# Optimization experiments

Hardware: AMD Instinct MI355X
Metric: run time of the kernel (lower is better)

The kernel has to match this reference:

```python
import jax, jax.numpy as jnp
import numpy as np

N_NODES = 50000
N_EDGES = 800000
IN_F = 128
OUT_F = 128
N_LAYERS = 2


def setup_inputs() -> dict:
    key = jax.random.key(0)
    ks = jax.random.split(key, 8)
    x = jax.random.normal(ks[0], (N_NODES, IN_F), dtype=jnp.float32)
    hidden_states = jax.random.normal(ks[1], (N_LAYERS, N_NODES, OUT_F), dtype=jnp.float32)
    src = jax.random.randint(ks[2], (N_EDGES,), 0, N_NODES)
    dst = jax.random.randint(ks[3], (N_EDGES,), 0, N_NODES)
    edge_w = jax.random.uniform(ks[4], (N_EDGES,), dtype=jnp.float32)
    # [layer, gate(r,u,c), in+out, out], scaled like typical init
    W_self = jax.random.normal(ks[5], (N_LAYERS, 3, IN_F + OUT_F, OUT_F), dtype=jnp.float32) * 0.05
    W_neigh = jax.random.normal(ks[6], (N_LAYERS, 3, IN_F + OUT_F, OUT_F), dtype=jnp.float32) * 0.05
    bias = jax.random.uniform(ks[7], (N_LAYERS, 3, OUT_F), dtype=jnp.float32)
    return {"x": x, "hidden_states": hidden_states, "src": src, "dst": dst,
            "edge_w": edge_w, "W_self": W_self, "W_neigh": W_neigh, "bias": bias}


def _gconv(z, src, dst, edge_w, ws, wn):
    # z: [N, 2F]; message passing: sum_{e: dst=v} edge_w[e] * z[src[e]]
    msg = z[src] * edge_w[:, None]                      # [E, 2F]
    agg = jax.ops.segment_sum(msg, dst, num_segments=N_NODES)  # [N, 2F]
    return z @ ws + agg @ wn                            # [N, F]


def _cell(x, h, src, dst, edge_w, ws, wn, b):
    # ws/wn: [3, 2F, F], b: [3, F]; gates r,u,c as in GraphGRUCell
    xh = jnp.concatenate([x, h], axis=1)
    r = jax.nn.sigmoid(_gconv(xh, src, dst, edge_w, ws[0], wn[0]) + b[0])
    u = jax.nn.sigmoid(_gconv(xh, src, dst, edge_w, ws[1], wn[1]) + b[1])
    xh2 = jnp.concatenate([x, r * h], axis=1)
    c = jax.nn.sigmoid(_gconv(xh2, src, dst, edge_w, ws[2], wn[2]) + b[2])
    return u * h + (1.0 - u) * c


def reference(x, hidden_states, src, dst, edge_w, W_self, W_neigh, bias):
    hiddens = []
    for i in range(N_LAYERS):  # small fixed layer count
        x = _cell(x, hidden_states[i], src, dst, edge_w, W_self[i], W_neigh[i], bias[i])
        hiddens.append(x)
    return (x, hiddens)
```

## Files before the change

kernel.cpp:

```cpp
#include <hip/hip_runtime.h>
#include <math.h>

#define F 128
#define NLAYERS 2

typedef __attribute__((ext_vector_type(8))) short bf16x8s;
typedef __attribute__((ext_vector_type(8))) unsigned short u16x8;
typedef __attribute__((ext_vector_type(4))) float f32x4;

__device__ __forceinline__ float sigmoidf_(float x) { return 1.0f / (1.0f + expf(-x)); }

__device__ __forceinline__ unsigned short f2bf(float f) {
    unsigned int u = __float_as_uint(f);
    u += 0x7fffu + ((u >> 16) & 1u);
    return (unsigned short)(u >> 16);
}
__device__ __forceinline__ float bf2f(unsigned short s) {
    return __uint_as_float(((unsigned int)s) << 16);
}

__global__ void pack_w_bf16(const float* __restrict__ Ws, const float* __restrict__ Wn,
                            unsigned short* __restrict__ W1b, unsigned short* __restrict__ W2b) {
    int t = blockIdx.x * blockDim.x + threadIdx.x;
    const int n1 = 2 * 64 * 256 * 8;
    if (t < n1) {
        int j = t & 7, n = (t >> 3) & 255, ko = (t >> 11) & 63, l = t >> 17;
        int k = ko * 8 + j;
        int p = k >> 7, r = k & 127, g = n >> 7, c = n & 127;
        const float* W = (p < 2) ? Ws : Wn;
        W1b[t] = f2bf(W[(((l * 3 + g) * 256) + ((p & 1) * 128 + r)) * 128 + c]);
    } else {
        int t2 = t - n1;
        if (t2 >= 2 * 64 * 128 * 8) return;
        int j = t2 & 7, n = (t2 >> 3) & 127, ko = (t2 >> 10) & 63, l = t2 >> 16;
        int k = ko * 8 + j;
        int p = k >> 7, r = k & 127;
        const float* W = (p < 2) ? Ws : Wn;
        W2b[t2] = f2bf(W[(((l * 3 + 2) * 256) + ((p & 1) * 128 + r)) * 128 + n]);
    }
}

__global__ void cvt_all(const float* __restrict__ x, const float* __restrict__ hidden,
                        unsigned short* __restrict__ xh0, unsigned short* __restrict__ xh1,
                        int n4, size_t NF) {
    int t = blockIdx.x * blockDim.x + threadIdx.x;
    const float* in;
    unsigned short* out;
    int tt;
    if (t < n4) { in = x; out = xh0; tt = t; }
    else if (t < 2 * n4) { in = hidden; out = xh0 + 128; tt = t - n4; }
    else if (t < 3 * n4) { in = hidden + NF; out = xh1 + 128; tt = t - 2 * n4; }
    else return;
    float4 v = reinterpret_cast<const float4*>(in)[tt];
    ushort4 o;
    o.x = f2bf(v.x); o.y = f2bf(v.y); o.z = f2bf(v.z); o.w = f2bf(v.w);
    *reinterpret_cast<ushort4*>(out + (((size_t)(tt >> 5)) << 8) + ((tt & 31) << 2)) = o;
}

__global__ void hist_key(const int* __restrict__ src, const int* __restrict__ dst,
                         int* __restrict__ cnt, int E) {
    int e = blockIdx.x * blockDim.x + threadIdx.x;
    if (e < E) atomicAdd(&cnt[(dst[e] << 4) + (src[e] >> 12)], 1);
}

__global__ __launch_bounds__(1024) void scan_blk(const int* __restrict__ cnt,
                                                 int* __restrict__ offs,
                                                 int* __restrict__ bsum, int n) {
    __shared__ int wsum[16];
    int tid = threadIdx.x, lane = tid & 63, wid = tid >> 6;
    int i = blockIdx.x * 1024 + tid;
    int v = (i < n) ? cnt[i] : 0;
    int incl = v;
#pragma unroll
    for (int off = 1; off < 64; off <<= 1) {
        int t = __shfl_up(incl, off, 64);
        if (lane >= off) incl += t;
    }
    if (lane == 63) wsum[wid] = incl;
    __syncthreads();
    if (wid == 0) {
        int s = (lane < 16) ? wsum[lane] : 0;
#pragma unroll
        for (int off = 1; off < 16; off <<= 1) {
            int t = __shfl_up(s, off, 64);
            if (lane >= off) s += t;
        }
        if (lane < 16) wsum[lane] = s;
    }
    __syncthreads();
    int wbase = (wid > 0) ? wsum[wid - 1] : 0;
    if (i < n) offs[i] = wbase + incl - v;
    if (tid == 1023) bsum[blockIdx.x] = wbase + incl;
}

__global__ __launch_bounds__(1024) void scan_tops(int* __restrict__ bsum, int nb,
                                                  int* __restrict__ total_out) {
    __shared__ int wsum[16];
    int tid = threadIdx.x, lane = tid & 63, wid = tid >> 6;
    int v = (tid < nb) ? bsum[tid] : 0;
    int incl = v;
#pragma unroll
    for (int off = 1; off < 64; off <<= 1) {
        int t = __shfl_up(incl, off, 64);
        if (lane >= off) incl += t;
    }
    if (lane == 63) wsum[wid] = incl;
    __syncthreads();
    if (wid == 0) {
        int s = (lane < 16) ? wsum[lane] : 0;
#pragma unroll
        for (int off = 1; off < 16; off <<= 1) {
            int t = __shfl_up(s, off, 64);
            if (lane >= off) s += t;
        }
        if (lane < 16) wsum[lane] = s;
    }
    __syncthreads();
    int wbase = (wid > 0) ? wsum[wid - 1] : 0;
    if (tid < nb) bsum[tid] = wbase + incl - v;
    if (tid == 1023) *total_out = wbase + incl;
}

__global__ __launch_bounds__(1024) void scan_add(const int* __restrict__ bsum,
                                                 int* __restrict__ offs,
                                                 int* __restrict__ cursor, int n) {
    int i = blockIdx.x * 1024 + threadIdx.x;
    if (i >= n) return;
    int o = offs[i] + bsum[blockIdx.x];
    offs[i] = o;
    cursor[i] = o;
}

__global__ void scatter_edges(const int* __restrict__ src, const int* __restrict__ dst,
                              const float* __restrict__ ew, int* __restrict__ cursor,
                              int2* __restrict__ es, int E) {
    int e = blockIdx.x * blockDim.x + threadIdx.x;
    if (e >= E) return;
    int s = src[e];
    int key = (dst[e] << 4) + (s >> 12);
    int p = atomicAdd(&cursor[key], 1);
    es[p] = make_int2(s, __float_as_int(ew[e]));
}

__global__ __launch_bounds__(256) void agg_csr2_i(
    const unsigned short* __restrict__ XH,
    const int2* __restrict__ es, const int* __restrict__ offs2,
    unsigned short* __restrict__ agg0, unsigned short* __restrict__ agg1, int N) {
    int node = blockIdx.x * 8 + (threadIdx.x >> 5);
    if (node >= N) return;
    int lane = threadIdx.x & 31;
    int beg = offs2[node << 4], end = offs2[(node << 4) + 16];
    float a0[8] = {0, 0, 0, 0, 0, 0, 0, 0};
    float a1[8] = {0, 0, 0, 0, 0, 0, 0, 0};
    int loff = lane << 3;
    int i = beg;
    for (; i + 3 < end; i += 4) {
        int2 e0 = es[i], e1 = es[i + 1], e2 = es[i + 2], e3 = es[i + 3];
        u16x8 v0 = *reinterpret_cast<const u16x8*>(XH + (((size_t)e0.x) << 8) + loff);
        u16x8 v1 = *reinterpret_cast<const u16x8*>(XH + (((size_t)e1.x) << 8) + loff);
        u16x8 v2 = *reinterpret_cast<const u16x8*>(XH + (((size_t)e2.x) << 8) + loff);
        u16x8 v3 = *reinterpret_cast<const u16x8*>(XH + (((size_t)e3.x) << 8) + loff);
        float w0 = __int_as_float(e0.y), w1 = __int_as_float(e1.y);
        float w2 = __int_as_float(e2.y), w3 = __int_as_float(e3.y);
#pragma unroll
        for (int j = 0; j < 8; ++j) {
            a0[j] += w0 * bf2f(v0[j]);
            a1[j] += w1 * bf2f(v1[j]);
            a0[j] += w2 * bf2f(v2[j]);
            a1[j] += w3 * bf2f(v3[j]);
        }
    }
    for (; i < end; ++i) {
        int2 e0 = es[i];
        float w0 = __int_as_float(e0.y);
        u16x8 v0 = *reinterpret_cast<const u16x8*>(XH + (((size_t)e0.x) << 8) + loff);
#pragma unroll
        for (int j = 0; j < 8; ++j) a0[j] += w0 * bf2f(v0[j]);
    }
    u16x8 o;
#pragma unroll
    for (int j = 0; j < 8; ++j) o[j] = f2bf(a0[j] + a1[j]);
    unsigned short* op = (lane < 16)
        ? (agg0 + (((size_t)node) << 7) + (lane << 3))
        : (agg1 + (((size_t)node) << 7) + ((lane & 15) << 3));
    *reinterpret_cast<u16x8*>(op) = o;
}

__global__ __launch_bounds__(256) void agg_csr1_b(
    const unsigned short* __restrict__ V0,
    const int2* __restrict__ es, const int* __restrict__ offs2,
    unsigned short* __restrict__ agg0, int N) {
    int node = blockIdx.x * 8 + (threadIdx.x >> 5);
    if (node >= N) return;
    int lane = threadIdx.x & 31;
    int beg = offs2[node << 4], end = offs2[(node << 4) + 16];
    float p0[4] = {0, 0, 0, 0}, p1[4] = {0, 0, 0, 0};
    int loff = lane << 2;
    int i = beg;
    for (; i + 3 < end; i += 4) {
        int2 e0 = es[i], e1 = es[i + 1], e2 = es[i + 2], e3 = es[i + 3];
        ushort4 x0 = *reinterpret_cast<const ushort4*>(V0 + (((size_t)e0.x) << 7) + loff);
        ushort4 x1 = *reinterpret_cast<const ushort4*>(V0 + (((size_t)e1.x) << 7) + loff);
        ushort4 x2 = *reinterpret_cast<const ushort4*>(V0 + (((size_t)e2.x) << 7) + loff);
        ushort4 x3 = *reinterpret_cast<const ushort4*>(V0 + (((size_t)e3.x) << 7) + loff);
        float w0 = __int_as_float(e0.y), w1 = __int_as_float(e1.y);
        float w2 = __int_as_float(e2.y), w3 = __int_as_float(e3.y);
        p0[0] += w0 * bf2f(x0.x); p0[1] += w0 * bf2f(x0.y);
        p0[2] += w0 * bf2f(x0.z); p0[3] += w0 * bf2f(x0.w);
        p1[0] += w1 * bf2f(x1.x); p1[1] += w1 * bf2f(x1.y);
        p1[2] += w1 * bf2f(x1.z); p1[3] += w1 * bf2f(x1.w);
        p0[0] += w2 * bf2f(x2.x); p0[1] += w2 * bf2f(x2.y);
        p0[2] += w2 * bf2f(x2.z); p0[3] += w2 * bf2f(x2.w);
        p1[0] += w3 * bf2f(x3.x); p1[1] += w3 * bf2f(x3.y);
        p1[2] += w3 * bf2f(x3.z); p1[3] += w3 * bf2f(x3.w);
    }
    for (; i < end; ++i) {
        int2 e0 = es[i];
        float w0 = __int_as_float(e0.y);
        ushort4 x0 = *reinterpret_cast<const ushort4*>(V0 + (((size_t)e0.x) << 7) + loff);
        p0[0] += w0 * bf2f(x0.x); p0[1] += w0 * bf2f(x0.y);
        p0[2] += w0 * bf2f(x0.z); p0[3] += w0 * bf2f(x0.w);
    }
    size_t ob = (((size_t)node) << 7) + loff;
    ushort4 o0;
    o0.x = f2bf(p0[0] + p1[0]); o0.y = f2bf(p0[1] + p1[1]);
    o0.z = f2bf(p0[2] + p1[2]); o0.w = f2bf(p0[3] + p1[3]);
    *reinterpret_cast<ushort4*>(agg0 + ob) = o0;
}

__global__ __launch_bounds__(512) void gemm_ru(
    const unsigned short* __restrict__ XH,
    const unsigned short* __restrict__ AGGX, const unsigned short* __restrict__ AGGH,
    const unsigned short* __restrict__ Wb, const float* __restrict__ bias,
    const float* __restrict__ hfull,
    unsigned short* __restrict__ rhb, float* __restrict__ u, int N) {
    __shared__ __align__(16) unsigned short Als[2][4 * 128 * 8];
    __shared__ __align__(16) unsigned short Bls[2][4 * 128 * 8];

    int tid = threadIdx.x;
    int row0 = blockIdx.x * 128;
    int n0c = blockIdx.y * 128;
    int lane = tid & 63;
    int w = tid >> 6;
    int wrow = (w & 1) << 6;
    int wcol = (w >> 1) << 5;
    int quad = lane >> 4, l16 = lane & 15;

    f32x4 acc[4][2];
    const f32x4 z4 = {0.f, 0.f, 0.f, 0.f};
#pragma unroll
    for (int mt = 0; mt < 4; ++mt)
#pragma unroll
        for (int nt = 0; nt < 2; ++nt) acc[mt][nt] = z4;

    int mA = tid & 127, qA = tid >> 7;
    int growA = row0 + mA;
    if (growA >= N) growA = N - 1;
    int nB = tid & 127, qB = tid >> 7;

    auto stage = [&](int ks, int buf) {
        int p = ks >> 7;
        const unsigned short* ga =
            (p == 0) ? (XH + (size_t)growA * 256 + (ks & 127) + (qA << 3))
          : (p == 1) ? (XH + (size_t)growA * 256 + 128 + (ks & 127) + (qA << 3))
          : (p == 2) ? (AGGX + ((size_t)growA << 7) + (ks & 127) + (qA << 3))
                     : (AGGH + ((size_t)growA << 7) + (ks & 127) + (qA << 3));
        __builtin_amdgcn_global_load_lds(
            (const __attribute__((address_space(1))) void*)ga,
            (__attribute__((address_space(3))) void*)&Als[buf][((qA << 7) + mA) << 3], 16, 0, 0);
        int koG = (ks >> 3) + qB;
        const unsigned short* gb = Wb + ((size_t)(koG * 256 + n0c + nB) << 3);
        __builtin_amdgcn_global_load_lds(
            (const __attribute__((address_space(1))) void*)gb,
            (__attribute__((address_space(3))) void*)&Bls[buf][((qB << 7) + nB) << 3], 16, 0, 0);
    };

    stage(0, 0);
    __syncthreads();
    int buf = 0;
    for (int ks = 0; ks < 512; ks += 32, buf ^= 1) {
        if (ks + 32 < 512) stage(ks + 32, buf ^ 1);

        bf16x8s af[4], bfr[2];
#pragma unroll
        for (int mt = 0; mt < 4; ++mt)
            af[mt] = *reinterpret_cast<const bf16x8s*>(
                &Als[buf][((quad << 7) + wrow + (mt << 4) + l16) << 3]);
#pragma unroll
        for (int nt = 0; nt < 2; ++nt)
            bfr[nt] = *reinterpret_cast<const bf16x8s*>(
                &Bls[buf][((quad << 7) + wcol + (nt << 4) + l16) << 3]);
#pragma unroll
        for (int mt = 0; mt < 4; ++mt)
#pragma unroll
            for (int nt = 0; nt < 2; ++nt)
                acc[mt][nt] = __builtin_amdgcn_mfma_f32_16x16x32_bf16(
                    af[mt], bfr[nt], acc[mt][nt], 0, 0, 0);
        __syncthreads();
    }

#pragma unroll
    for (int mt = 0; mt < 4; ++mt) {
#pragma unroll
        for (int reg = 0; reg < 4; ++reg) {
            int row = row0 + wrow + (mt << 4) + (quad << 2) + reg;
            if (row >= N) continue;
#pragma unroll
            for (int nt = 0; nt < 2; ++nt) {
                int col = n0c + wcol + (nt << 4) + l16;
                float val = acc[mt][nt][reg] + bias[col];
                float sg = sigmoidf_(val);
                int c = col & 127;
                size_t o = ((size_t)row << 7) + c;
                if (col < 128)
                    rhb[o] = f2bf(sg * hfull[o]);
                else
                    u[o] = sg;
            }
        }
    }
}

__global__ __launch_bounds__(512) void gemm_c(
    const unsigned short* __restrict__ XH, const unsigned short* __restrict__ RHB,
    const unsigned short* __restrict__ AGGX, const unsigned short* __restrict__ AGGR,
    const unsigned short* __restrict__ Wb, const float* __restrict__ bias,
    const float* __restrict__ hfull, const float* __restrict__ uin,
    unsigned short* __restrict__ outb, float* __restrict__ outf,
    float* __restrict__ outf2, int obsh, int N) {
    __shared__ __align__(16) unsigned short Als[2][4 * 128 * 8];
    __shared__ __align__(16) unsigned short Bls[2][4 * 128 * 8];

    int tid = threadIdx.x;
    int row0 = blockIdx.x * 128;
    int lane = tid & 63;
    int w = tid >> 6;
    int wrow = (w & 1) << 6;
    int wcol = (w >> 1) << 5;
    int quad = lane >> 4, l16 = lane & 15;

    f32x4 acc[4][2];
    const f32x4 z4 = {0.f, 0.f, 0.f, 0.f};
#pragma unroll
    for (int mt = 0; mt < 4; ++mt)
#pragma unroll
        for (int nt = 0; nt < 2; ++nt) acc[mt][nt] = z4;

    int mA = tid & 127, qA = tid >> 7;
    int growA = row0 + mA;
    if (growA >= N) growA = N - 1;
    int nB = tid & 127, qB = tid >> 7;

    auto stage = [&](int ks, int buf) {
        int p = ks >> 7;
        const unsigned short* ga =
            (p == 0) ? (XH + (size_t)growA * 256 + (ks & 127) + (qA << 3))
          : (p == 1) ? (RHB + ((size_t)growA << 7) + (ks & 127) + (qA << 3))
          : (p == 2) ? (AGGX + ((size_t)growA << 7) + (ks & 127) + (qA << 3))
                     : (AGGR + ((size_t)growA << 7) + (ks & 127) + (qA << 3));
        __builtin_amdgcn_global_load_lds(
            (const __attribute__((address_space(1))) void*)ga,
            (__attribute__((address_space(3))) void*)&Als[buf][((qA << 7) + mA) << 3], 16, 0, 0);
        int koG = (ks >> 3) + qB;
        const unsigned short* gb = Wb + ((size_t)(koG * 128 + nB) << 3);
        __builtin_amdgcn_global_load_lds(
            (const __attribute__((address_space(1))) void*)gb,
            (__attribute__((address_space(3))) void*)&Bls[buf][((qB << 7) + nB) << 3], 16, 0, 0);
    };

    stage(0, 0);
    __syncthreads();
    int buf = 0;
    for (int ks = 0; ks < 512; ks += 32, buf ^= 1) {
        if (ks + 32 < 512) stage(ks + 32, buf ^ 1);

        bf16x8s af[4], bfr[2];
#pragma unroll
        for (int mt = 0; mt < 4; ++mt)
            af[mt] = *reinterpret_cast<const bf16x8s*>(
                &Als[buf][((quad << 7) + wrow + (mt << 4) + l16) << 3]);
#pragma unroll
        for (int nt = 0; nt < 2; ++nt)
            bfr[nt] = *reinterpret_cast<const bf16x8s*>(
                &Bls[buf][((quad << 7) + wcol + (nt << 4) + l16) << 3]);
#pragma unroll
        for (int mt = 0; mt < 4; ++mt)
#pragma unroll
            for (int nt = 0; nt < 2; ++nt)
                acc[mt][nt] = __builtin_amdgcn_mfma_f32_16x16x32_bf16(
                    af[mt], bfr[nt], acc[mt][nt], 0, 0, 0);
        __syncthreads();
    }

#pragma unroll
    for (int mt = 0; mt < 4; ++mt) {
#pragma unroll
        for (int reg = 0; reg < 4; ++reg) {
            int row = row0 + wrow + (mt << 4) + (quad << 2) + reg;
            if (row >= N) continue;
#pragma unroll
            for (int nt = 0; nt < 2; ++nt) {
                int col = wcol + (nt << 4) + l16;
                float val = acc[mt][nt][reg] + bias[col];
                float cv = sigmoidf_(val);
                size_t o = ((size_t)row << 7) + col;
                float uu = uin[o];
                float hh = hfull[o];
                float hn = uu * hh + (1.0f - uu) * cv;
                outf[o] = hn;
                if (outf2) outf2[o] = hn;
                outb[((size_t)row << obsh) + col] = f2bf(hn);
            }
        }
    }
}

extern "C" void kernel_launch(void* const* d_in, const int* in_sizes, int n_in,
                              void* d_out, int out_size, void* d_ws, size_t ws_size,
                              hipStream_t stream) {
    const float* x      = (const float*)d_in[0];
    const float* hidden = (const float*)d_in[1];
    const int*   src    = (const int*)d_in[2];
    const int*   dst    = (const int*)d_in[3];
    const float* ew     = (const float*)d_in[4];
    const float* Wself  = (const float*)d_in[5];
    const float* Wneigh = (const float*)d_in[6];
    const float* bias   = (const float*)d_in[7];
    float* out = (float*)d_out;

    int N = in_sizes[0] / F;
    int E = in_sizes[2];
    size_t NF = (size_t)N * F;
    int NK = N * 16;

    char* p = (char*)d_ws;
    auto alloc = [&](size_t bytes) { char* r = p; p += (bytes + 255) & ~255ull; return r; };
    unsigned short* xh0    = (unsigned short*)alloc(2 * NF * 2);
    unsigned short* xh1    = (unsigned short*)alloc(2 * NF * 2);
    unsigned short* agg_xb = (unsigned short*)alloc(NF * 2);
    unsigned short* agg_hb = (unsigned short*)alloc(NF * 2);
    unsigned short* agg_rb = (unsigned short*)alloc(NF * 2);
    unsigned short* rhb    = (unsigned short*)alloc(NF * 2);
    float*          u      = (float*)alloc(NF * 4);
    unsigned short* W1b    = (unsigned short*)alloc(2 * 64 * 256 * 8 * 2);
    unsigned short* W2b    = (unsigned short*)alloc(2 * 64 * 128 * 8 * 2);
    int2*           es     = (int2*)alloc((size_t)E * 8);
    int*            cnt2   = (int*)alloc((size_t)NK * 4);
    int*            offs2  = (int*)alloc(((size_t)NK + 1) * 4);
    int*            cur2   = (int*)alloc((size_t)NK * 4);
    int*            bsum   = (int*)alloc(1024 * 4);

    pack_w_bf16<<<dim3(1536), dim3(256), 0, stream>>>(Wself, Wneigh, W1b, W2b);
    int n4 = (int)(NF / 4);
    cvt_all<<<dim3((3 * n4 + 255) / 256), dim3(256), 0, stream>>>(x, hidden, xh0, xh1, n4, NF);

    hipMemsetAsync(cnt2, 0, (size_t)NK * sizeof(int), stream);
    int eBlocks = (E + 255) / 256;
    hist_key<<<dim3(eBlocks), dim3(256), 0, stream>>>(src, dst, cnt2, E);
    int nb = (NK + 1023) / 1024;
    scan_blk<<<dim3(nb), dim3(1024), 0, stream>>>(cnt2, offs2, bsum, NK);
    scan_tops<<<dim3(1), dim3(1024), 0, stream>>>(bsum, nb, offs2 + NK);
    scan_add<<<dim3(nb), dim3(1024), 0, stream>>>(bsum, offs2, cur2, NK);
    scatter_edges<<<dim3(eBlocks), dim3(256), 0, stream>>>(src, dst, ew, cur2, es, E);

    float* out_x  = out;
    float* out_h1 = out + NF;
    float* out_h2 = out + 2 * NF;

    int aggBlocks = (N + 7) / 8;
    int mBlocks = (N + 127) / 128;
    for (int l = 0; l < NLAYERS; ++l) {
        unsigned short* xhL = (l == 0) ? xh0 : xh1;
        const float* hL = hidden + (size_t)l * NF;
        const float* biasL = bias + (size_t)l * 384;

        agg_csr2_i<<<dim3(aggBlocks), dim3(256), 0, stream>>>(xhL, es, offs2,
                                                              agg_xb, agg_hb, N);

        gemm_ru<<<dim3(mBlocks, 2), dim3(512), 0, stream>>>(
            xhL, agg_xb, agg_hb,
            W1b + (size_t)l * 64 * 256 * 8, biasL, hL,
            rhb, u, N);

        agg_csr1_b<<<dim3(aggBlocks), dim3(256), 0, stream>>>(rhb, es, offs2, agg_rb, N);

        float* o1 = (l == 0) ? out_h1 : out_h2;
        float* o2 = (l == NLAYERS - 1) ? out_x : nullptr;
        unsigned short* obN = (l == 0) ? xh1 : agg_rb;
        int obsh = (l == 0) ? 8 : 7;
        gemm_c<<<dim3(mBlocks), dim3(512), 0, stream>>>(
            xhL, rhb, agg_xb, agg_rb,
            W2b + (size_t)l * 64 * 128 * 8, biasL + 256, hL, u,
            obN, o1, o2, obsh, N);
    }
}
```

Measured before the change: 588.4 us.

## Fuse prologue kernels and drop src-bucketed CSR keys for plain per-node CSR

Measured after the change: 590.0 us. Within noise of the previous version (+0.3%).

```diff
diff --git a/kernel.cpp b/kernel.cpp
--- a/kernel.cpp
+++ b/kernel.cpp
@@ -19,48 +19,56 @@
     return __uint_as_float(((unsigned int)s) << 16);
 }
 
-__global__ void pack_w_bf16(const float* __restrict__ Ws, const float* __restrict__ Wn,
-                            unsigned short* __restrict__ W1b, unsigned short* __restrict__ W2b) {
-    int t = blockIdx.x * blockDim.x + threadIdx.x;
-    const int n1 = 2 * 64 * 256 * 8;
-    if (t < n1) {
-        int j = t & 7, n = (t >> 3) & 255, ko = (t >> 11) & 63, l = t >> 17;
-        int k = ko * 8 + j;
-        int p = k >> 7, r = k & 127, g = n >> 7, c = n & 127;
-        const float* W = (p < 2) ? Ws : Wn;
-        W1b[t] = f2bf(W[(((l * 3 + g) * 256) + ((p & 1) * 128 + r)) * 128 + c]);
+__global__ void prologue(const float* __restrict__ x, const float* __restrict__ hidden,
+                         const float* __restrict__ Ws, const float* __restrict__ Wn,
+                         const int* __restrict__ dst,
+                         unsigned short* __restrict__ xh0, unsigned short* __restrict__ xh1,
+                         unsigned short* __restrict__ W1b, unsigned short* __restrict__ W2b,
+                         int* __restrict__ cnt, int n4, size_t NF, int E, int cvtBlocks) {
+    int b = blockIdx.x;
+    int tid = threadIdx.x;
+    if (b < cvtBlocks) {
+        int t = b * 256 + tid;
+        const float* in;
+        unsigned short* out;
+        int tt;
+        if (t < n4) { in = x; out = xh0; tt = t; }
+        else if (t < 2 * n4) { in = hidden; out = xh0 + 128; tt = t - n4; }
+        else if (t < 3 * n4) { in = hidden + NF; out = xh1 + 128; tt = t - 2 * n4; }
+        else return;
+        float4 v = reinterpret_cast<const float4*>(in)[tt];
+        ushort4 o;
+        o.x = f2bf(v.x); o.y = f2bf(v.y); o.z = f2bf(v.z); o.w = f2bf(v.w);
+        *reinterpret_cast<ushort4*>(out + (((size_t)(tt >> 5)) << 8) + ((tt & 31) << 2)) = o;
+    } else if (b < cvtBlocks + 1536) {
+        int t = (b - cvtBlocks) * 256 + tid;
+        const int n1 = 2 * 64 * 256 * 8;
+        if (t < n1) {
+            int j = t & 7, n = (t >> 3) & 255, ko = (t >> 11) & 63, l = t >> 17;
+            int k = ko * 8 + j;
+            int p = k >> 7, r = k & 127, g = n >> 7, c = n & 127;
+            const float* W = (p < 2) ? Ws : Wn;
+            W1b[t] = f2bf(W[(((l * 3 + g) * 256) + ((p & 1) * 128 + r)) * 128 + c]);
+        } else {
+            int t2 = t - n1;
+            if (t2 >= 2 * 64 * 128 * 8) return;
+            int j = t2 & 7, n = (t2 >> 3) & 127, ko = (t2 >> 10) & 63, l = t2 >> 16;
+            int k = ko * 8 + j;
+            int p = k >> 7, r = k & 127;
+            const float* W = (p < 2) ? Ws : Wn;
+            W2b[t2] = f2bf(W[(((l * 3 + 2) * 256) + ((p & 1) * 128 + r)) * 128 + n]);
+        }
     } else {
-        int t2 = t - n1;
-        if (t2 >= 2 * 64 * 128 * 8) return;
-        int j = t2 & 7, n = (t2 >> 3) & 127, ko = (t2 >> 10) & 63, l = t2 >> 16;
-        int k = ko * 8 + j;
-        int p = k >> 7, r = k & 127;
-        const float* W = (p < 2) ? Ws : Wn;
-        W2b[t2] = f2bf(W[(((l * 3 + 2) * 256) + ((p & 1) * 128 + r)) * 128 + n]);
-    }
-}
-
-__global__ void cvt_all(const float* __restrict__ x, const float* __restrict__ hidden,
-                        unsigned short* __restrict__ xh0, unsigned short* __restrict__ xh1,
-                        int n4, size_t NF) {
-    int t = blockIdx.x * blockDim.x + threadIdx.x;
-    const float* in;
-    unsigned short* out;
-    int tt;
-    if (t < n4) { in = x; out = xh0; tt = t; }
-    else if (t < 2 * n4) { in = hidden; out = xh0 + 128; tt = t - n4; }
-    else if (t < 3 * n4) { in = hidden + NF; out = xh1 + 128; tt = t - 2 * n4; }
-    else return;
-    float4 v = reinterpret_cast<const float4*>(in)[tt];
-    ushort4 o;
-    o.x = f2bf(v.x); o.y = f2bf(v.y); o.z = f2bf(v.z); o.w = f2bf(v.w);
-    *reinterpret_cast<ushort4*>(out + (((size_t)(tt >> 5)) << 8) + ((tt & 31) << 2)) = o;
-}
-
-__global__ void hist_key(const int* __restrict__ src, const int* __restrict__ dst,
-                         int* __restrict__ cnt, int E) {
-    int e = blockIdx.x * blockDim.x + threadIdx.x;
-    if (e < E) atomicAdd(&cnt[(dst[e] << 4) + (src[e] >> 12)], 1);
+        int t = (b - cvtBlocks - 1536) * 256 + tid;
+        int e = t << 1;
+        if (e + 1 < E) {
+            int2 d = *reinterpret_cast<const int2*>(dst + e);
+            atomicAdd(&cnt[d.x], 1);
+            atomicAdd(&cnt[d.y], 1);
+        } else if (e < E) {
+            atomicAdd(&cnt[dst[e]], 1);
+        }
+    }
 }
 
 __global__ __launch_bounds__(1024) void scan_blk(const int* __restrict__ cnt,
@@ -134,22 +142,31 @@
 __global__ void scatter_edges(const int* __restrict__ src, const int* __restrict__ dst,
                               const float* __restrict__ ew, int* __restrict__ cursor,
                               int2* __restrict__ es, int E) {
-    int e = blockIdx.x * blockDim.x + threadIdx.x;
-    if (e >= E) return;
-    int s = src[e];
-    int key = (dst[e] << 4) + (s >> 12);
-    int p = atomicAdd(&cursor[key], 1);
-    es[p] = make_int2(s, __float_as_int(ew[e]));
+    int t = blockIdx.x * blockDim.x + threadIdx.x;
+    int e = t << 1;
+    if (e + 1 < E) {
+        int2 s = *reinterpret_cast<const int2*>(src + e);
+        int2 d = *reinterpret_cast<const int2*>(dst + e);
+        float2 w = *reinterpret_cast<const float2*>(ew + e);
+        int p0 = atomicAdd(&cursor[d.x], 1);
+        int p1 = atomicAdd(&cursor[d.y], 1);
+        es[p0] = make_int2(s.x, __float_as_int(w.x));
+        es[p1] = make_int2(s.y, __float_as_int(w.y));
+    } else if (e < E) {
+        int s = src[e];
+        int p = atomicAdd(&cursor[dst[e]], 1);
+        es[p] = make_int2(s, __float_as_int(ew[e]));
+    }
 }
 
 __global__ __launch_bounds__(256) void agg_csr2_i(
     const unsigned short* __restrict__ XH,
-    const int2* __restrict__ es, const int* __restrict__ offs2,
+    const int2* __restrict__ es, const int* __restrict__ offs,
     unsigned short* __restrict__ agg0, unsigned short* __restrict__ agg1, int N) {
     int node = blockIdx.x * 8 + (threadIdx.x >> 5);
     if (node >= N) return;
     int lane = threadIdx.x & 31;
-    int beg = offs2[node << 4], end = offs2[(node << 4) + 16];
+    int beg = offs[node], end = offs[node + 1];
     float a0[8] = {0, 0, 0, 0, 0, 0, 0, 0};
     float a1[8] = {0, 0, 0, 0, 0, 0, 0, 0};
     int loff = lane << 3;
@@ -188,12 +205,12 @@
 
 __global__ __launch_bounds__(256) void agg_csr1_b(
     const unsigned short* __restrict__ V0,
-    const int2* __restrict__ es, const int* __restrict__ offs2,
+    const int2* __restrict__ es, const int* __restrict__ offs,
     unsigned short* __restrict__ agg0, int N) {
     int node = blockIdx.x * 8 + (threadIdx.x >> 5);
     if (node >= N) return;
     int lane = threadIdx.x & 31;
-    int beg = offs2[node << 4], end = offs2[(node << 4) + 16];
+    int beg = offs[node], end = offs[node + 1];
     float p0[4] = {0, 0, 0, 0}, p1[4] = {0, 0, 0, 0};
     int loff = lane << 2;
     int i = beg;
@@ -431,7 +448,6 @@
     int N = in_sizes[0] / F;
     int E = in_sizes[2];
     size_t NF = (size_t)N * F;
-    int NK = N * 16;
 
     char* p = (char*)d_ws;
     auto alloc = [&](size_t bytes) { char* r = p; p += (bytes + 255) & ~255ull; return r; };
@@ -445,23 +461,25 @@
     unsigned short* W1b    = (unsigned short*)alloc(2 * 64 * 256 * 8 * 2);
     unsigned short* W2b    = (unsigned short*)alloc(2 * 64 * 128 * 8 * 2);
     int2*           es     = (int2*)alloc((size_t)E * 8);
-    int*            cnt2   = (int*)alloc((size_t)NK * 4);
-    int*            offs2  = (int*)alloc(((size_t)NK + 1) * 4);
-    int*            cur2   = (int*)alloc((size_t)NK * 4);
+    int*            cnt    = (int*)alloc((size_t)N * 4);
+    int*            offs   = (int*)alloc(((size_t)N + 1) * 4);
+    int*            cursor = (int*)alloc((size_t)N * 4);
     int*            bsum   = (int*)alloc(1024 * 4);
 
-    pack_w_bf16<<<dim3(1536), dim3(256), 0, stream>>>(Wself, Wneigh, W1b, W2b);
+    hipMemsetAsync(cnt, 0, (size_t)N * sizeof(int), stream);
+
     int n4 = (int)(NF / 4);
-    cvt_all<<<dim3((3 * n4 + 255) / 256), dim3(256), 0, stream>>>(x, hidden, xh0, xh1, n4, NF);
-
-    hipMemsetAsync(cnt2, 0, (size_t)NK * sizeof(int), stream);
-    int eBlocks = (E + 255) / 256;
-    hist_key<<<dim3(eBlocks), dim3(256), 0, stream>>>(src, dst, cnt2, E);
-    int nb = (NK + 1023) / 1024;
-    scan_blk<<<dim3(nb), dim3(1024), 0, stream>>>(cnt2, offs2, bsum, NK);
-    scan_tops<<<dim3(1), dim3(1024), 0, stream>>>(bsum, nb, offs2 + NK);
-    scan_add<<<dim3(nb), dim3(1024), 0, stream>>>(bsum, offs2, cur2, NK);
-    scatter_edges<<<dim3(eBlocks), dim3(256), 0, stream>>>(src, dst, ew, cur2, es, E);
+    int cvtBlocks = (3 * n4 + 255) / 256;
+    int histBlocks = (E / 2 + 255) / 256;
+    prologue<<<dim3(cvtBlocks + 1536 + histBlocks), dim3(256), 0, stream>>>(
+        x, hidden, Wself, Wneigh, dst, xh0, xh1, W1b, W2b, cnt, n4, NF, E, cvtBlocks);
+
+    int nb = (N + 1023) / 1024;
+    scan_blk<<<dim3(nb), dim3(1024), 0, stream>>>(cnt, offs, bsum, N);
+    scan_tops<<<dim3(1), dim3(1024), 0, stream>>>(bsum, nb, offs + N);
+    scan_add<<<dim3(nb), dim3(1024), 0, stream>>>(bsum, offs, cursor, N);
+    int e2Blocks = (E / 2 + 255) / 256;
+    scatter_edges<<<dim3(e2Blocks), dim3(256), 0, stream>>>(src, dst, ew, cursor, es, E);
 
     float* out_x  = out;
     float* out_h1 = out + NF;
@@ -474,7 +492,7 @@
         const float* hL = hidden + (size_t)l * NF;
         const float* biasL = bias + (size_t)l * 384;
 
-        agg_csr2_i<<<dim3(aggBlocks), dim3(256), 0, stream>>>(xhL, es, offs2,
+        agg_csr2_i<<<dim3(aggBlocks), dim3(256), 0, stream>>>(xhL, es, offs,
                                                               agg_xb, agg_hb, N);
 
         gemm_ru<<<dim3(mBlocks, 2), dim3(512), 0, stream>>>(
@@ -482,7 +500,7 @@
             W1b + (size_t)l * 64 * 256 * 8, biasL, hL,
             rhb, u, N);
 
-        agg_csr1_b<<<dim3(aggBlocks), dim3(256), 0, stream>>>(rhb, es, offs2, agg_rb, N);
+        agg_csr1_b<<<dim3(aggBlocks), dim3(256), 0, stream>>>(rhb, es, offs, agg_rb, N);
 
         float* o1 = (l == 0) ? out_h1 : out_h2;
         float* o2 = (l == NLAYERS - 1) ? out_x : nullptr;
```
